# Optimization experiments

Hardware: AMD Instinct MI355X
Metric: run time of the kernel (lower is better)

Reference implementation:

```python
import jax, jax.numpy as jnp
import numpy as np

B, GRID, CIN, COUT, TDIM, NMODES = 32, 128, 32, 32, 256, 32
M = NMODES // 2 + 1  # kept modes per axis = 17
FFT_NORM = 'forward'


def setup_inputs() -> dict:
    key = jax.random.key(0)
    ks = jax.random.split(key, 10)
    w_std = float(np.sqrt(1.0 / (2.0 * CIN)))          # normal_initializer(in_co_dim)
    k_std = float(np.sqrt(1.0 / TDIM))                 # ~lecun_normal for Dense kernels
    wshape = (M, M, CIN, COUT)
    return {
        'x': jax.random.normal(ks[0], (B, GRID, GRID, CIN), jnp.float32),
        't_emb': jax.random.normal(ks[1], (B, TDIM), jnp.float32),
        'w1_real': w_std * jax.random.normal(ks[2], wshape, jnp.float32),
        'w1_imag': w_std * jax.random.normal(ks[3], wshape, jnp.float32),
        'w2_real': w_std * jax.random.normal(ks[4], wshape, jnp.float32),
        'w2_imag': w_std * jax.random.normal(ks[5], wshape, jnp.float32),
        'k1_real': k_std * jax.random.normal(ks[6], (TDIM, M), jnp.float32),
        'k1_imag': k_std * jax.random.normal(ks[7], (TDIM, M), jnp.float32),
        'k2_real': k_std * jax.random.normal(ks[8], (TDIM, M), jnp.float32),
        'k2_imag': k_std * jax.random.normal(ks[9], (TDIM, M), jnp.float32),
    }


def reference(x, t_emb, w1_real, w1_imag, w2_real, w2_imag,
              k1_real, k1_imag, k2_real, k2_imag):
    b, n = x.shape[0], x.shape[1]
    # rFFT2 over spatial axes: (b, n, n//2+1, cin) complex
    x_ft = jnp.fft.rfft2(x, axes=(1, 2), norm=FFT_NORM)

    w1 = w1_real + 1j * w1_imag  # (M, M, cin, cout)
    w2 = w2_real + 1j * w2_imag
    # Time modulation: Dense(no bias) -> complex per-mode scale t[b, i].
    # The original builds diag(t) and einsums it into the weights; that equals a
    # simple broadcast scale over the first mode axis, fused here.
    t1 = (t_emb @ k1_real) + 1j * (t_emb @ k1_imag)  # (b, M)
    t2 = (t_emb @ k2_real) + 1j * (t_emb @ k2_imag)

    # Mode-truncated complex channel contraction, scaled by t along axis i.
    xf1 = jnp.einsum('bijc,ijco->bijo', x_ft[:, :M, :M, :], w1) * t1[:, :, None, None]
    xf2 = jnp.einsum('bijc,ijco->bijo', x_ft[:, -M:, :M, :], w2) * t2[:, :, None, None]

    out_ft = jnp.zeros((b, n, n // 2 + 1, COUT), dtype=jnp.complex64)
    out_ft = out_ft.at[:, :M, :M, :].set(xf1)
    out_ft = out_ft.at[:, -M:, :M, :].set(xf2)

    return jnp.fft.irfft2(out_ft, s=(n, n), axes=(1, 2), norm=FFT_NORM)
```

## Files before the change

kernel.cpp:

```cpp
#include <hip/hip_runtime.h>
#include <stdint.h>


#define TWO_PI_OVER_128 0.04908738521234052f

__global__ __launch_bounds__(128) void k_tproj(
    const float* __restrict__ temb, const float* __restrict__ k1r, const float* __restrict__ k1i,
    const float* __restrict__ k2r, const float* __restrict__ k2i, float* __restrict__ tbuf)
{
    int b = blockIdx.x, tid = threadIdx.x;
    __shared__ float ts[256];
    for (int d = tid; d < 256; d += 128) ts[d] = temb[b * 256 + d];
    __syncthreads();
    if (tid < 68) {
        int which = (tid >= 34) ? 1 : 0;
        int rem = tid - which * 34;
        int i = rem >> 1, part = rem & 1;
        const float* kp = which ? (part ? k2i : k2r) : (part ? k1i : k1r);
        float acc = 0.f;
        for (int d = 0; d < 256; ++d) acc += ts[d] * kp[d * 17 + i];
        tbuf[((which * 32 + b) * 17 + i) * 2 + part] = acc;
    }
}

__global__ __launch_bounds__(64) void k_fwd_y(const float* __restrict__ x, float2* __restrict__ T1)
{
    int blk = blockIdx.x;
    int b = blk >> 7, xr = blk & 127;
    __shared__ float xs[128 * 32];
    int tid = threadIdx.x;
    const float4* xv = (const float4*)(x + ((size_t)blk << 12));
    float4* xs4 = (float4*)xs;
#pragma unroll
    for (int i = 0; i < 16; ++i) xs4[tid + (i << 6)] = xv[tid + (i << 6)];
    __syncthreads();
    for (int i = tid; i < 2016; i += 64) {
        int y = (i >> 5) + 1, c = i & 31;
        float a = xs[(y << 5) + c], q = xs[((128 - y) << 5) + c];
        xs[(y << 5) + c] = a + q;
        xs[((128 - y) << 5) + c] = a - q;
    }
    __syncthreads();
    int jg = tid >> 3, cg = tid & 7, c0 = cg << 2;
    float re[2][4] = {{0,0,0,0},{0,0,0,0}}, im[2][4] = {{0,0,0,0},{0,0,0,0}};
    float stc[2], sts[2], cr[2], ci[2];
#pragma unroll
    for (int t = 0; t < 2; ++t) {
        int j = jg + t * 8;
        float sn, cs; sincosf(TWO_PI_OVER_128 * (float)j, &sn, &cs);
        stc[t] = cs; sts[t] = -sn; cr[t] = cs; ci[t] = -sn;
    }
    for (int y = 1; y <= 63; ++y) {
        float4 s = *(const float4*)&xs[(y << 5) + c0];
        float4 d = *(const float4*)&xs[((128 - y) << 5) + c0];
#pragma unroll
        for (int t = 0; t < 2; ++t) {
            re[t][0] = fmaf(s.x, cr[t], re[t][0]);
            re[t][1] = fmaf(s.y, cr[t], re[t][1]);
            re[t][2] = fmaf(s.z, cr[t], re[t][2]);
            re[t][3] = fmaf(s.w, cr[t], re[t][3]);
            im[t][0] = fmaf(d.x, ci[t], im[t][0]);
            im[t][1] = fmaf(d.y, ci[t], im[t][1]);
            im[t][2] = fmaf(d.z, ci[t], im[t][2]);
            im[t][3] = fmaf(d.w, ci[t], im[t][3]);
            float nr = cr[t] * stc[t] - ci[t] * sts[t];
            ci[t] = fmaf(cr[t], sts[t], ci[t] * stc[t]);
            cr[t] = nr;
        }
    }
    const float s_ = 1.f / 16384.f;
    float x0[4], x64[4];
    *(float4*)x0  = *(const float4*)&xs[c0];
    *(float4*)x64 = *(const float4*)&xs[(64 << 5) + c0];
#pragma unroll
    for (int t = 0; t < 2; ++t) {
        int j = jg + t * 8;
        float sg = (j & 1) ? -1.f : 1.f;
        float2* p = T1 + (((size_t)(b * 17 + j) * 128 + xr) << 5) + c0;
        float4 v0 = make_float4((re[t][0] + x0[0] + sg * x64[0]) * s_, im[t][0] * s_,
                                (re[t][1] + x0[1] + sg * x64[1]) * s_, im[t][1] * s_);
        float4 v1 = make_float4((re[t][2] + x0[2] + sg * x64[2]) * s_, im[t][2] * s_,
                                (re[t][3] + x0[3] + sg * x64[3]) * s_, im[t][3] * s_);
        ((float4*)p)[0] = v0; ((float4*)p)[1] = v1;
    }
    if (jg == 0) {
        float re2[4] = {0,0,0,0}, im2[4] = {0,0,0,0};
        const float cs = 0.7071067811865476f, sn = -0.7071067811865476f;
        float cr2 = cs, ci2 = sn;
        for (int y = 1; y <= 63; ++y) {
            float4 s = *(const float4*)&xs[(y << 5) + c0];
            float4 d = *(const float4*)&xs[((128 - y) << 5) + c0];
            re2[0] = fmaf(s.x, cr2, re2[0]); re2[1] = fmaf(s.y, cr2, re2[1]);
            re2[2] = fmaf(s.z, cr2, re2[2]); re2[3] = fmaf(s.w, cr2, re2[3]);
            im2[0] = fmaf(d.x, ci2, im2[0]); im2[1] = fmaf(d.y, ci2, im2[1]);
            im2[2] = fmaf(d.z, ci2, im2[2]); im2[3] = fmaf(d.w, ci2, im2[3]);
            float nr = cr2 * cs - ci2 * sn;
            ci2 = fmaf(cr2, sn, ci2 * cs);
            cr2 = nr;
        }
        float2* p = T1 + (((size_t)(b * 17 + 16) * 128 + xr) << 5) + c0;
        float4 v0 = make_float4((re2[0] + x0[0] + x64[0]) * s_, im2[0] * s_,
                                (re2[1] + x0[1] + x64[1]) * s_, im2[1] * s_);
        float4 v1 = make_float4((re2[2] + x0[2] + x64[2]) * s_, im2[2] * s_,
                                (re2[3] + x0[3] + x64[3]) * s_, im2[3] * s_);
        ((float4*)p)[0] = v0; ((float4*)p)[1] = v1;
    }
}

__global__ __launch_bounds__(512) void k_mid_fused(
    const float2* __restrict__ T1, const float* __restrict__ w1r, const float* __restrict__ w1i,
    const float* __restrict__ w2r, const float* __restrict__ w2i,
    const float* __restrict__ tbuf, float2* __restrict__ U)
{
    int blk = blockIdx.x;
    int b = blk / 17, j = blk - b * 17;
    __shared__ float4 Ts4[2048];
    __shared__ float2 Xf[34 * 32];
    __shared__ float ct[128], st[128];
    int tid = threadIdx.x;
    const float4* s4 = (const float4*)(T1 + (size_t)blk * 4096);
    for (int i = tid; i < 2048; i += 512) Ts4[i] = s4[i];
    if (tid < 128) {
        float a = TWO_PI_OVER_128 * (float)tid;
        sincosf(a, &st[tid], &ct[tid]);
    }
    __syncthreads();
    for (int i = tid; i < 1008; i += 512) {
        int x = (i >> 4) + 1, cp = i & 15;
        float4 a = Ts4[(x << 4) + cp], q = Ts4[((128 - x) << 4) + cp];
        Ts4[(x << 4) + cp] = make_float4(a.x + q.x, a.y + q.y, a.z + q.z, a.w + q.w);
        Ts4[((128 - x) << 4) + cp] = make_float4(a.x - q.x, a.y - q.y, a.z - q.z, a.w - q.w);
    }
    __syncthreads();
    {
        int cp = tid & 15, g = tid >> 4;
        if (g < 16) {
            int f = g + 1;
            float sn, cs; sincosf(TWO_PI_OVER_128 * (float)f, &sn, &cs);
            float cr = cs, ci = sn;
            float P0=0,Q0=0,R0=0,T0=0,P1=0,Q1=0,R1=0,T1a=0;
            for (int x = 1; x <= 63; ++x) {
                float4 S = Ts4[(x << 4) + cp];
                float4 D = Ts4[((128 - x) << 4) + cp];
                P0 = fmaf(S.x, cr, P0); Q0 = fmaf(D.y, ci, Q0);
                R0 = fmaf(S.y, cr, R0); T0 = fmaf(D.x, ci, T0);
                P1 = fmaf(S.z, cr, P1); Q1 = fmaf(D.w, ci, Q1);
                R1 = fmaf(S.w, cr, R1); T1a = fmaf(D.z, ci, T1a);
                float nr = cr * cs - ci * sn;
                ci = fmaf(cr, sn, ci * cs);
                cr = nr;
            }
            float4 t0 = Ts4[cp], t64 = Ts4[(64 << 4) + cp];
            float sg = (f & 1) ? -1.f : 1.f;
            float b0r = t0.x + sg * t64.x, b0i = t0.y + sg * t64.y;
            float b1r = t0.z + sg * t64.z, b1i = t0.w + sg * t64.w;
            int ia = f, ib = 34 - f;
            Xf[ia * 32 + cp*2]   = make_float2(P0 + Q0 + b0r, R0 - T0 + b0i);
            Xf[ia * 32 + cp*2+1] = make_float2(P1 + Q1 + b1r, R1 - T1a + b1i);
            Xf[ib * 32 + cp*2]   = make_float2(P0 - Q0 + b0r, R0 + T0 + b0i);
            Xf[ib * 32 + cp*2+1] = make_float2(P1 - Q1 + b1r, R1 + T1a + b1i);
            if (g == 0) {
                float A0=0,B0=0,A1=0,B1=0;
                for (int x = 1; x <= 63; ++x) {
                    float4 S = Ts4[(x << 4) + cp];
                    A0 += S.x; B0 += S.y; A1 += S.z; B1 += S.w;
                }
                Xf[cp*2]   = make_float2(A0 + t0.x + t64.x, B0 + t0.y + t64.y);
                Xf[cp*2+1] = make_float2(A1 + t0.z + t64.z, B1 + t0.w + t64.w);
            }
            if (g == 8) {
                float sn2, cs2; sincosf(TWO_PI_OVER_128 * 111.f, &sn2, &cs2);
                float cr2 = cs2, ci2 = sn2;
                float p0=0,q0=0,r0=0,s0=0,p1=0,q1=0,r1=0,s1=0;
                for (int x = 1; x <= 63; ++x) {
                    float4 S = Ts4[(x << 4) + cp];
                    float4 D = Ts4[((128 - x) << 4) + cp];
                    p0 = fmaf(S.x, cr2, p0); q0 = fmaf(D.y, ci2, q0);
                    r0 = fmaf(S.y, cr2, r0); s0 = fmaf(D.x, ci2, s0);
                    p1 = fmaf(S.z, cr2, p1); q1 = fmaf(D.w, ci2, q1);
                    r1 = fmaf(S.w, cr2, r1); s1 = fmaf(D.z, ci2, s1);
                    float nr = cr2 * cs2 - ci2 * sn2;
                    ci2 = fmaf(cr2, sn2, ci2 * cs2);
                    cr2 = nr;
                }
                float c0r = t0.x - t64.x, c0i = t0.y - t64.y;
                float c1r = t0.z - t64.z, c1i = t0.w - t64.w;
                Xf[17*32 + cp*2]   = make_float2(p0 + q0 + c0r, r0 - s0 + c0i);
                Xf[17*32 + cp*2+1] = make_float2(p1 + q1 + c1r, r1 - s1 + c1i);
            }
        }
    }
    __syncthreads();
    float2* Ys = (float2*)Ts4;
    {
        int o = tid & 31, gi = tid >> 5;
#pragma unroll
        for (int t = 0; t < 3; ++t) {
            int ii = gi + (t << 4);
            if (ii < 34) {
                int irow = (ii < 17) ? ii : ii - 17;
                const float* wr = ((ii < 17) ? w1r : w2r) + ((irow * 17 + j) << 10) + o;
                const float* wi = ((ii < 17) ? w1i : w2i) + ((irow * 17 + j) << 10) + o;
                float ar = 0.f, ai = 0.f;
#pragma unroll 8
                for (int c = 0; c < 32; ++c) {
                    float2 xv = Xf[ii * 32 + c];
                    float wre = wr[c << 5], wim = wi[c << 5];
                    ar += xv.x * wre - xv.y * wim;
                    ai += xv.x * wim + xv.y * wre;
                }
                int which = (ii >= 17) ? 1 : 0;
                const float* tp = tbuf + ((which * 32 + b) * 17 + irow) * 2;
                float tr = tp[0], ti = tp[1];
                Ys[ii * 32 + o] = make_float2(ar * tr - ai * ti, ar * ti + ai * tr);
            }
        }
    }
    __syncthreads();
    {
        int o = tid & 31, g = tid >> 5;
        float yr[34], yi[34];
#pragma unroll
        for (int i = 0; i < 34; ++i) { float2 v = Ys[i * 32 + o]; yr[i] = v.x; yi[i] = v.y; }
        float2* Ub = U + ((size_t)b * 128 * 17 + j) * 32 + o;
        if (g == 0) {
            float sr = 0.f, si = 0.f;
#pragma unroll
            for (int i = 0; i < 34; ++i) { sr += yr[i]; si += yi[i]; }
            Ub[0] = make_float2(sr, si);
        }
        for (int k = 0; k < 4; ++k) {
            int x = 1 + g + (k << 4);
            if (x == 64) {
                float sr = 0.f, si = 0.f;
#pragma unroll
                for (int i = 0; i < 34; ++i) {
                    float sg2 = (i & 1) ? -1.f : 1.f;
                    sr = fmaf(sg2, yr[i], sr); si = fmaf(sg2, yi[i], si);
                }
                Ub[(size_t)64 * 544] = make_float2(sr, si);
            } else {
                float cx = ct[x], sx = st[x];
                float A1=0,A2=0,A3=0,A4=0;
                float cr = 1.f, ci = 0.f;
#pragma unroll
                for (int i = 0; i < 17; ++i) {
                    A1 = fmaf(yr[i], cr, A1); A4 = fmaf(yr[i], ci, A4);
                    A3 = fmaf(yi[i], cr, A3); A2 = fmaf(yi[i], ci, A2);
                    float nr = cr * cx - ci * sx;
                    ci = fmaf(cr, sx, ci * cx);
                    cr = nr;
                }
                int k2 = (111 * x) & 127;
                cr = ct[k2]; ci = st[k2];
#pragma unroll
                for (int i = 17; i < 34; ++i) {
                    A1 = fmaf(yr[i], cr, A1); A4 = fmaf(yr[i], ci, A4);
                    A3 = fmaf(yi[i], cr, A3); A2 = fmaf(yi[i], ci, A2);
                    float nr = cr * cx - ci * sx;
                    ci = fmaf(cr, sx, ci * cx);
                    cr = nr;
                }
                Ub[(size_t)x * 544]         = make_float2(A1 - A2, A3 + A4);
                Ub[(size_t)(128 - x) * 544] = make_float2(A1 + A2, A3 - A4);
            }
        }
    }
}

__global__ __launch_bounds__(256) void k_fwd_x_mix(
    const float2* __restrict__ T1, const float* __restrict__ w1r, const float* __restrict__ w1i,
    const float* __restrict__ w2r, const float* __restrict__ w2i,
    const float* __restrict__ tbuf, float2* __restrict__ Y)
{
    int blk = blockIdx.x;
    int b = blk / 17, j = blk - b * 17;
    __shared__ float4 Ts4[2048];
    __shared__ float2 Xf[34 * 32];
    int tid = threadIdx.x;
    const float4* s4 = (const float4*)(T1 + (size_t)blk * 4096);
    for (int i = tid; i < 2048; i += 256) Ts4[i] = s4[i];
    __syncthreads();
    {
        int cp = tid & 15, g = tid >> 4;
        int il[3] = {g, g + 16, g + 32};
        float stc[3], sts[3];
#pragma unroll
        for (int t = 0; t < 3; ++t) {
            int i = il[t];
            int f = (i < 17) ? i : i + 94;
            float a = -TWO_PI_OVER_128 * (float)(f & 127);
            sincosf(a, &sts[t], &stc[t]);
        }
        float cr[3] = {1.f, 1.f, 1.f}, ci[3] = {0.f, 0.f, 0.f};
        float r0[3] = {0,0,0}, i0[3] = {0,0,0}, r1[3] = {0,0,0}, i1[3] = {0,0,0};
        const float4* Tc = Ts4 + cp;
#pragma unroll 2
        for (int xx = 0; xx < 128; ++xx) {
            float4 tv = Tc[xx << 4];
#pragma unroll
            for (int t = 0; t < 3; ++t) {
                r0[t] += tv.x * cr[t] - tv.y * ci[t];
                i0[t] += tv.x * ci[t] + tv.y * cr[t];
                r1[t] += tv.z * cr[t] - tv.w * ci[t];
                i1[t] += tv.z * ci[t] + tv.w * cr[t];
                float nr = cr[t] * stc[t] - ci[t] * sts[t];
                ci[t] = fmaf(cr[t], sts[t], ci[t] * stc[t]);
                cr[t] = nr;
            }
        }
#pragma unroll
        for (int t = 0; t < 3; ++t) {
            int i = il[t];
            if (i < 34) {
                Xf[i * 32 + cp * 2]     = make_float2(r0[t], i0[t]);
                Xf[i * 32 + cp * 2 + 1] = make_float2(r1[t], i1[t]);
            }
        }
    }
    __syncthreads();
    {
        int o = tid & 31, gi = tid >> 5;
#pragma unroll
        for (int t = 0; t < 5; ++t) {
            int ii = gi + (t << 3);
            if (ii < 34) {
                int irow = (ii < 17) ? ii : ii - 17;
                const float* wr = ((ii < 17) ? w1r : w2r) + ((irow * 17 + j) << 10) + o;
                const float* wi = ((ii < 17) ? w1i : w2i) + ((irow * 17 + j) << 10) + o;
                float ar = 0.f, ai = 0.f;
#pragma unroll 8
                for (int cc2 = 0; cc2 < 32; ++cc2) {
                    float2 xv = Xf[ii * 32 + cc2];
                    float wre = wr[cc2 << 5];
                    float wim = wi[cc2 << 5];
                    ar += xv.x * wre - xv.y * wim;
                    ai += xv.x * wim + xv.y * wre;
                }
                int which = (ii >= 17) ? 1 : 0;
                const float* tp = tbuf + ((which * 32 + b) * 17 + irow) * 2;
                float tr = tp[0], ti = tp[1];
                Y[(size_t)blk * (34 * 32) + ii * 32 + o] =
                    make_float2(ar * tr - ai * ti, ar * ti + ai * tr);
            }
        }
    }
}

__global__ __launch_bounds__(256) void k_inv_x(const float2* __restrict__ Y, float2* __restrict__ U)
{
    int blk = blockIdx.x;
    int b = blk / 17, j = blk - b * 17;
    __shared__ float2 Ys[34 * 32];
    __shared__ float ct[128], st[128];
    int tid = threadIdx.x;
    if (tid < 128) {
        float a = TWO_PI_OVER_128 * (float)tid;
        sincosf(a, &st[tid], &ct[tid]);
    }
    const float2* src = Y + (size_t)blk * (34 * 32);
    for (int i = tid; i < 34 * 32; i += 256) Ys[i] = src[i];
    __syncthreads();
    int o = tid & 31, g = tid >> 5;
    float yr[34], yi[34];
#pragma unroll
    for (int i = 0; i < 34; ++i) { float2 v = Ys[i * 32 + o]; yr[i] = v.x; yi[i] = v.y; }
    for (int xi = 0; xi < 16; ++xi) {
        int xr = (xi << 3) + g;
        float cx = ct[xr], sx = st[xr];
        float cr = 1.f, ci = 0.f, re = 0.f, im = 0.f;
#pragma unroll
        for (int i = 0; i < 17; ++i) {
            re += yr[i] * cr - yi[i] * ci;
            im += yr[i] * ci + yi[i] * cr;
            float nr = cr * cx - ci * sx;
            ci = fmaf(cr, sx, ci * cx);
            cr = nr;
        }
        int k2 = (111 * xr) & 127;
        cr = ct[k2]; ci = st[k2];
#pragma unroll
        for (int i = 17; i < 34; ++i) {
            re += yr[i] * cr - yi[i] * ci;
            im += yr[i] * ci + yi[i] * cr;
            float nr = cr * cx - ci * sx;
            ci = fmaf(cr, sx, ci * cx);
            cr = nr;
        }
        U[(((size_t)(b * 128 + xr)) * 17 + j) * 32 + o] = make_float2(re, im);
    }
}

__global__ __launch_bounds__(128) void k_inv_y(const float2* __restrict__ U, float* __restrict__ out)
{
    int blk = blockIdx.x;
    __shared__ float2 Us[17 * 32];
    int tid = threadIdx.x;
    const float4* src4 = (const float4*)(U + (size_t)blk * 544);
    float4* Us4 = (float4*)Us;
    for (int i = tid; i < 272; i += 128) Us4[i] = src4[i];
    __syncthreads();
    int cg = tid & 15, yg = tid >> 4, c0 = cg << 1;
    float base0, base1;
    {
        float4 v = *(const float4*)&Us[c0];
        base0 = v.x; base1 = v.z;
    }
    float urr[16][2], uii[16][2];
#pragma unroll
    for (int j = 1; j <= 16; ++j) {
        float4 v = *(const float4*)&Us[j * 32 + c0];
        urr[j-1][0] = 2.f * v.x; uii[j-1][0] = 2.f * v.y;
        urr[j-1][1] = 2.f * v.z; uii[j-1][1] = 2.f * v.w;
    }
    float* op = out + ((size_t)blk << 12);
    for (int k = 0; k < 9; ++k) {
        int y = yg + (k << 3);
        if (y > 64) break;
        float cy, sy; sincosf(TWO_PI_OVER_128 * (float)y, &sy, &cy);
        float cr = cy, ci = sy;
        float A0 = 0.f, A1 = 0.f, B0 = 0.f, B1 = 0.f;
#pragma unroll
        for (int j = 0; j < 16; ++j) {
            A0 = fmaf(urr[j][0], cr, A0);
            B0 = fmaf(uii[j][0], ci, B0);
            A1 = fmaf(urr[j][1], cr, A1);
            B1 = fmaf(uii[j][1], ci, B1);
            float nr = cr * cy - ci * sy;
            ci = fmaf(cr, sy, ci * cy);
            cr = nr;
        }
        *(float2*)&op[(y << 5) + c0] = make_float2(base0 + A0 - B0, base1 + A1 - B1);
        if (y > 0 && y < 64)
            *(float2*)&op[((128 - y) << 5) + c0] = make_float2(base0 + A0 + B0, base1 + A1 + B1);
    }
}

extern "C" void kernel_launch(void* const* d_in, const int* in_sizes, int n_in,
                              void* d_out, int out_size, void* d_ws, size_t ws_size,
                              hipStream_t stream)
{
    const float* x    = (const float*)d_in[0];
    const float* temb = (const float*)d_in[1];
    const float* w1r  = (const float*)d_in[2];
    const float* w1i  = (const float*)d_in[3];
    const float* w2r  = (const float*)d_in[4];
    const float* w2i  = (const float*)d_in[5];
    const float* k1r  = (const float*)d_in[6];
    const float* k1i  = (const float*)d_in[7];
    const float* k2r  = (const float*)d_in[8];
    const float* k2i  = (const float*)d_in[9];
    float* out = (float*)d_out;

    char* ws = (char*)d_ws;
    const size_t T1_BYTES = 17825792;
    const size_t NEED_FUSED = 2 * T1_BYTES + 8704;

    if (ws_size >= NEED_FUSED) {
        float2* T1 = (float2*)ws;
        float2* U  = (float2*)(ws + T1_BYTES);
        float*  tb = (float*)(ws + 2 * T1_BYTES);
        k_tproj    <<<32,   128, 0, stream>>>(temb, k1r, k1i, k2r, k2i, tb);
        k_fwd_y    <<<4096, 64,  0, stream>>>(x, T1);
        k_mid_fused<<<544,  512, 0, stream>>>(T1, w1r, w1i, w2r, w2i, tb, U);
        k_inv_y    <<<4096, 128, 0, stream>>>(U, out);
    } else {
        float2* T1 = (float2*)ws;
        float2* Yb = (float2*)(ws + T1_BYTES);
        float*  tb = (float*)(ws + T1_BYTES + 4734976);
        float2* U  = T1;
        k_tproj    <<<32,   128, 0, stream>>>(temb, k1r, k1i, k2r, k2i, tb);
        k_fwd_y    <<<4096, 64,  0, stream>>>(x, T1);
        k_fwd_x_mix<<<544,  256, 0, stream>>>(T1, w1r, w1i, w2r, w2i, tb, Yb);
        k_inv_x    <<<544,  256, 0, stream>>>(Yb, U);
        k_inv_y    <<<4096, 128, 0, stream>>>(U, out);
    }
}
```

Before: 213.0 us.

## Replace y-axis DFT stages with split-bf16 MFMA matrix multiplies against precomputed twiddle tables

Rewrites the forward and inverse y-axis DFT kernels as small GEMMs on MFMA units. Twiddle matrices are precomputed into bf16 hi/lo tables by a new single-block kernel, and three-term split-bf16 products approximate fp32 accuracy. The fallback path with separate x-mix and inverse-x kernels is removed, so a larger workspace is now always assumed. The aim is to move the scalar FMA recurrence work onto matrix cores, at the cost of an extra launch, table reads and some precision loss from the bf16 splitting.

Measured after the change: 213.7 us. No clear change (+0.3%).

```diff
diff --git a/kernel.cpp b/kernel.cpp
--- a/kernel.cpp
+++ b/kernel.cpp
@@ -2,7 +2,19 @@
 #include <stdint.h>
 
 
+typedef unsigned int uint32;
+typedef __attribute__((ext_vector_type(8))) short short8;
+typedef __attribute__((ext_vector_type(4))) float f32x4;
+
 #define TWO_PI_OVER_128 0.04908738521234052f
+
+__device__ __forceinline__ unsigned short bfhi(float v) {
+    uint32 u = __float_as_uint(v);
+    return (unsigned short)((u + 0x7fffu + ((u >> 16) & 1u)) >> 16);
+}
+__device__ __forceinline__ float bf2f(unsigned short h) {
+    return __uint_as_float(((uint32)h) << 16);
+}
 
 __global__ __launch_bounds__(128) void k_tproj(
     const float* __restrict__ temb, const float* __restrict__ k1r, const float* __restrict__ k1i,
@@ -23,87 +35,150 @@
     }
 }
 
-__global__ __launch_bounds__(64) void k_fwd_y(const float* __restrict__ x, float2* __restrict__ T1)
-{
-    int blk = blockIdx.x;
-    int b = blk >> 7, xr = blk & 127;
-    __shared__ float xs[128 * 32];
+__global__ __launch_bounds__(256) void k_mktab(
+    unsigned short* __restrict__ Dhi, unsigned short* __restrict__ Dlo,
+    unsigned short* __restrict__ Ehi, unsigned short* __restrict__ Elo,
+    float* __restrict__ Et)
+{
     int tid = threadIdx.x;
-    const float4* xv = (const float4*)(x + ((size_t)blk << 12));
-    float4* xs4 = (float4*)xs;
-#pragma unroll
-    for (int i = 0; i < 16; ++i) xs4[tid + (i << 6)] = xv[tid + (i << 6)];
-    __syncthreads();
-    for (int i = tid; i < 2016; i += 64) {
-        int y = (i >> 5) + 1, c = i & 31;
-        float a = xs[(y << 5) + c], q = xs[((128 - y) << 5) + c];
-        xs[(y << 5) + c] = a + q;
-        xs[((128 - y) << 5) + c] = a - q;
-    }
-    __syncthreads();
-    int jg = tid >> 3, cg = tid & 7, c0 = cg << 2;
-    float re[2][4] = {{0,0,0,0},{0,0,0,0}}, im[2][4] = {{0,0,0,0},{0,0,0,0}};
-    float stc[2], sts[2], cr[2], ci[2];
-#pragma unroll
-    for (int t = 0; t < 2; ++t) {
-        int j = jg + t * 8;
-        float sn, cs; sincosf(TWO_PI_OVER_128 * (float)j, &sn, &cs);
-        stc[t] = cs; sts[t] = -sn; cr[t] = cs; ci[t] = -sn;
-    }
-    for (int y = 1; y <= 63; ++y) {
-        float4 s = *(const float4*)&xs[(y << 5) + c0];
-        float4 d = *(const float4*)&xs[((128 - y) << 5) + c0];
-#pragma unroll
-        for (int t = 0; t < 2; ++t) {
-            re[t][0] = fmaf(s.x, cr[t], re[t][0]);
-            re[t][1] = fmaf(s.y, cr[t], re[t][1]);
-            re[t][2] = fmaf(s.z, cr[t], re[t][2]);
-            re[t][3] = fmaf(s.w, cr[t], re[t][3]);
-            im[t][0] = fmaf(d.x, ci[t], im[t][0]);
-            im[t][1] = fmaf(d.y, ci[t], im[t][1]);
-            im[t][2] = fmaf(d.z, ci[t], im[t][2]);
-            im[t][3] = fmaf(d.w, ci[t], im[t][3]);
-            float nr = cr[t] * stc[t] - ci[t] * sts[t];
-            ci[t] = fmaf(cr[t], sts[t], ci[t] * stc[t]);
-            cr[t] = nr;
-        }
-    }
-    const float s_ = 1.f / 16384.f;
-    float x0[4], x64[4];
-    *(float4*)x0  = *(const float4*)&xs[c0];
-    *(float4*)x64 = *(const float4*)&xs[(64 << 5) + c0];
-#pragma unroll
-    for (int t = 0; t < 2; ++t) {
-        int j = jg + t * 8;
-        float sg = (j & 1) ? -1.f : 1.f;
-        float2* p = T1 + (((size_t)(b * 17 + j) * 128 + xr) << 5) + c0;
-        float4 v0 = make_float4((re[t][0] + x0[0] + sg * x64[0]) * s_, im[t][0] * s_,
-                                (re[t][1] + x0[1] + sg * x64[1]) * s_, im[t][1] * s_);
-        float4 v1 = make_float4((re[t][2] + x0[2] + sg * x64[2]) * s_, im[t][2] * s_,
-                                (re[t][3] + x0[3] + sg * x64[3]) * s_, im[t][3] * s_);
-        ((float4*)p)[0] = v0; ((float4*)p)[1] = v1;
-    }
-    if (jg == 0) {
-        float re2[4] = {0,0,0,0}, im2[4] = {0,0,0,0};
-        const float cs = 0.7071067811865476f, sn = -0.7071067811865476f;
-        float cr2 = cs, ci2 = sn;
-        for (int y = 1; y <= 63; ++y) {
-            float4 s = *(const float4*)&xs[(y << 5) + c0];
-            float4 d = *(const float4*)&xs[((128 - y) << 5) + c0];
-            re2[0] = fmaf(s.x, cr2, re2[0]); re2[1] = fmaf(s.y, cr2, re2[1]);
-            re2[2] = fmaf(s.z, cr2, re2[2]); re2[3] = fmaf(s.w, cr2, re2[3]);
-            im2[0] = fmaf(d.x, ci2, im2[0]); im2[1] = fmaf(d.y, ci2, im2[1]);
-            im2[2] = fmaf(d.z, ci2, im2[2]); im2[3] = fmaf(d.w, ci2, im2[3]);
-            float nr = cr2 * cs - ci2 * sn;
-            ci2 = fmaf(cr2, sn, ci2 * cs);
-            cr2 = nr;
-        }
-        float2* p = T1 + (((size_t)(b * 17 + 16) * 128 + xr) << 5) + c0;
-        float4 v0 = make_float4((re2[0] + x0[0] + x64[0]) * s_, im2[0] * s_,
-                                (re2[1] + x0[1] + x64[1]) * s_, im2[1] * s_);
-        float4 v1 = make_float4((re2[2] + x0[2] + x64[2]) * s_, im2[2] * s_,
-                                (re2[3] + x0[3] + x64[3]) * s_, im2[3] * s_);
-        ((float4*)p)[0] = v0; ((float4*)p)[1] = v1;
+    for (int i = tid; i < 48 * 128; i += 256) {
+        int m = i >> 7, y = i & 127;
+        float v = 0.f;
+        if (m < 34) {
+            int p = m >> 1;
+            int k = (p * y) & 127;
+            float sn, cs; sincosf(TWO_PI_OVER_128 * (float)k, &sn, &cs);
+            v = ((m & 1) ? -sn : cs) * (1.f / 16384.f);
+        }
+        unsigned short h = bfhi(v);
+        Dhi[i] = h; Dlo[i] = bfhi(v - bf2f(h));
+    }
+    for (int i = tid; i < 128 * 32; i += 256) {
+        int y = i >> 5, q = i & 31;
+        int j = q >> 1;
+        int k = (j * y) & 127;
+        float sn, cs; sincosf(TWO_PI_OVER_128 * (float)k, &sn, &cs);
+        float w = (j == 0) ? 1.f : 2.f;
+        float v = (q & 1) ? (-w * sn) : (w * cs);
+        if (q == 1) v = 0.f;
+        unsigned short h = bfhi(v);
+        Ehi[i] = h; Elo[i] = bfhi(v - bf2f(h));
+    }
+    for (int i = tid; i < 128; i += 256) {
+        int k = (16 * i) & 127;
+        float sn, cs; sincosf(TWO_PI_OVER_128 * (float)k, &sn, &cs);
+        Et[i * 2] = 2.f * cs; Et[i * 2 + 1] = -2.f * sn;
+    }
+}
+
+__global__ __launch_bounds__(256) void k_fwd_y_mfma(
+    const float* __restrict__ x, float2* __restrict__ T1,
+    const unsigned short* __restrict__ Dhi, const unsigned short* __restrict__ Dlo)
+{
+    int wave = threadIdx.x >> 6, lane = threadIdx.x & 63;
+    int row = (blockIdx.x << 2) + wave;
+    int b = row >> 7, xr = row & 127;
+    const float* xp = x + ((size_t)row << 12);
+    int col = lane & 15, quad = lane >> 4;
+    f32x4 acc[3][2];
+#pragma unroll
+    for (int m = 0; m < 3; ++m)
+#pragma unroll
+        for (int n = 0; n < 2; ++n) acc[m][n] = (f32x4){0.f, 0.f, 0.f, 0.f};
+#pragma unroll
+    for (int t = 0; t < 4; ++t) {
+        int y0 = t * 32 + quad * 8;
+        short8 xh[2], xl[2];
+#pragma unroll
+        for (int n = 0; n < 2; ++n) {
+            const float* xc = xp + (n << 4) + col;
+#pragma unroll
+            for (int jj = 0; jj < 8; ++jj) {
+                float v = xc[(y0 + jj) << 5];
+                unsigned short h = bfhi(v);
+                xh[n][jj] = (short)h;
+                xl[n][jj] = (short)bfhi(v - bf2f(h));
+            }
+        }
+#pragma unroll
+        for (int m = 0; m < 3; ++m) {
+            int doff = (((m << 4) + col) << 7) + t * 32 + quad * 8;
+            short8 dh = *(const short8*)(Dhi + doff);
+            short8 dl = *(const short8*)(Dlo + doff);
+#pragma unroll
+            for (int n = 0; n < 2; ++n) {
+                acc[m][n] = __builtin_amdgcn_mfma_f32_16x16x32_bf16(dh, xh[n], acc[m][n], 0, 0, 0);
+                acc[m][n] = __builtin_amdgcn_mfma_f32_16x16x32_bf16(dh, xl[n], acc[m][n], 0, 0, 0);
+                acc[m][n] = __builtin_amdgcn_mfma_f32_16x16x32_bf16(dl, xh[n], acc[m][n], 0, 0, 0);
+            }
+        }
+    }
+#pragma unroll
+    for (int m = 0; m < 3; ++m) {
+        int j0 = (m << 3) + (quad << 1);
+#pragma unroll
+        for (int n = 0; n < 2; ++n) {
+            int c = (n << 4) + col;
+            if (m < 2 || quad == 0) {
+                float2* p = T1 + (((size_t)(b * 17 + j0) * 128 + xr) << 5) + c;
+                *p = make_float2(acc[m][n][0], acc[m][n][1]);
+            }
+            if (m < 2) {
+                float2* p = T1 + (((size_t)(b * 17 + j0 + 1) * 128 + xr) << 5) + c;
+                *p = make_float2(acc[m][n][2], acc[m][n][3]);
+            }
+        }
+    }
+}
+
+__global__ __launch_bounds__(256) void k_inv_y_mfma(
+    const float2* __restrict__ U, float* __restrict__ out,
+    const unsigned short* __restrict__ Ehi, const unsigned short* __restrict__ Elo,
+    const float* __restrict__ Et)
+{
+    int wave = threadIdx.x >> 6, lane = threadIdx.x & 63;
+    int row = (blockIdx.x << 2) + wave;
+    const float2* Up = U + (size_t)row * 544;
+    float* outp = out + ((size_t)row << 12);
+    int col = lane & 15, quad = lane >> 4;
+    short8 uh[2], ul[2];
+#pragma unroll
+    for (int n = 0; n < 2; ++n) {
+        int o = (n << 4) + col;
+#pragma unroll
+        for (int m = 0; m < 4; ++m) {
+            int j = (quad << 2) + m;
+            float2 uv = Up[(j << 5) + o];
+            unsigned short h0 = bfhi(uv.x);
+            uh[n][2 * m]     = (short)h0;
+            ul[n][2 * m]     = (short)bfhi(uv.x - bf2f(h0));
+            unsigned short h1 = bfhi(uv.y);
+            uh[n][2 * m + 1] = (short)h1;
+            ul[n][2 * m + 1] = (short)bfhi(uv.y - bf2f(h1));
+        }
+    }
+    float2 u16a = Up[(16 << 5) + col];
+    float2 u16b = Up[(16 << 5) + 16 + col];
+#pragma unroll
+    for (int mt = 0; mt < 8; ++mt) {
+        f32x4 a0 = (f32x4){0.f, 0.f, 0.f, 0.f};
+        f32x4 a1 = (f32x4){0.f, 0.f, 0.f, 0.f};
+        int eoff = (((mt << 4) + col) << 5) + (quad << 3);
+        short8 eh = *(const short8*)(Ehi + eoff);
+        short8 el = *(const short8*)(Elo + eoff);
+        a0 = __builtin_amdgcn_mfma_f32_16x16x32_bf16(eh, uh[0], a0, 0, 0, 0);
+        a0 = __builtin_amdgcn_mfma_f32_16x16x32_bf16(eh, ul[0], a0, 0, 0, 0);
+        a0 = __builtin_amdgcn_mfma_f32_16x16x32_bf16(el, uh[0], a0, 0, 0, 0);
+        a1 = __builtin_amdgcn_mfma_f32_16x16x32_bf16(eh, uh[1], a1, 0, 0, 0);
+        a1 = __builtin_amdgcn_mfma_f32_16x16x32_bf16(eh, ul[1], a1, 0, 0, 0);
+        a1 = __builtin_amdgcn_mfma_f32_16x16x32_bf16(el, uh[1], a1, 0, 0, 0);
+#pragma unroll
+        for (int r = 0; r < 4; ++r) {
+            int y = (mt << 4) + (quad << 2) + r;
+            float e0 = Et[y << 1], e1 = Et[(y << 1) + 1];
+            outp[(y << 5) + col]      = a0[r] + u16a.x * e0 + u16a.y * e1;
+            outp[(y << 5) + 16 + col] = a1[r] + u16b.x * e0 + u16b.y * e1;
+        }
     }
 }
 
@@ -268,174 +343,6 @@
     }
 }
 
-__global__ __launch_bounds__(256) void k_fwd_x_mix(
-    const float2* __restrict__ T1, const float* __restrict__ w1r, const float* __restrict__ w1i,
-    const float* __restrict__ w2r, const float* __restrict__ w2i,
-    const float* __restrict__ tbuf, float2* __restrict__ Y)
-{
-    int blk = blockIdx.x;
-    int b = blk / 17, j = blk - b * 17;
-    __shared__ float4 Ts4[2048];
-    __shared__ float2 Xf[34 * 32];
-    int tid = threadIdx.x;
-    const float4* s4 = (const float4*)(T1 + (size_t)blk * 4096);
-    for (int i = tid; i < 2048; i += 256) Ts4[i] = s4[i];
-    __syncthreads();
-    {
-        int cp = tid & 15, g = tid >> 4;
-        int il[3] = {g, g + 16, g + 32};
-        float stc[3], sts[3];
-#pragma unroll
-        for (int t = 0; t < 3; ++t) {
-            int i = il[t];
-            int f = (i < 17) ? i : i + 94;
-            float a = -TWO_PI_OVER_128 * (float)(f & 127);
-            sincosf(a, &sts[t], &stc[t]);
-        }
-        float cr[3] = {1.f, 1.f, 1.f}, ci[3] = {0.f, 0.f, 0.f};
-        float r0[3] = {0,0,0}, i0[3] = {0,0,0}, r1[3] = {0,0,0}, i1[3] = {0,0,0};
-        const float4* Tc = Ts4 + cp;
-#pragma unroll 2
-        for (int xx = 0; xx < 128; ++xx) {
-            float4 tv = Tc[xx << 4];
-#pragma unroll
-            for (int t = 0; t < 3; ++t) {
-                r0[t] += tv.x * cr[t] - tv.y * ci[t];
-                i0[t] += tv.x * ci[t] + tv.y * cr[t];
-                r1[t] += tv.z * cr[t] - tv.w * ci[t];
-                i1[t] += tv.z * ci[t] + tv.w * cr[t];
-                float nr = cr[t] * stc[t] - ci[t] * sts[t];
-                ci[t] = fmaf(cr[t], sts[t], ci[t] * stc[t]);
-                cr[t] = nr;
-            }
-        }
-#pragma unroll
-        for (int t = 0; t < 3; ++t) {
-            int i = il[t];
-            if (i < 34) {
-                Xf[i * 32 + cp * 2]     = make_float2(r0[t], i0[t]);
-                Xf[i * 32 + cp * 2 + 1] = make_float2(r1[t], i1[t]);
-            }
-        }
-    }
-    __syncthreads();
-    {
-        int o = tid & 31, gi = tid >> 5;
-#pragma unroll
-        for (int t = 0; t < 5; ++t) {
-            int ii = gi + (t << 3);
-            if (ii < 34) {
-                int irow = (ii < 17) ? ii : ii - 17;
-                const float* wr = ((ii < 17) ? w1r : w2r) + ((irow * 17 + j) << 10) + o;
-                const float* wi = ((ii < 17) ? w1i : w2i) + ((irow * 17 + j) << 10) + o;
-                float ar = 0.f, ai = 0.f;
-#pragma unroll 8
-                for (int cc2 = 0; cc2 < 32; ++cc2) {
-                    float2 xv = Xf[ii * 32 + cc2];
-                    float wre = wr[cc2 << 5];
-                    float wim = wi[cc2 << 5];
-                    ar += xv.x * wre - xv.y * wim;
-                    ai += xv.x * wim + xv.y * wre;
-                }
-                int which = (ii >= 17) ? 1 : 0;
-                const float* tp = tbuf + ((which * 32 + b) * 17 + irow) * 2;
-                float tr = tp[0], ti = tp[1];
-                Y[(size_t)blk * (34 * 32) + ii * 32 + o] =
-                    make_float2(ar * tr - ai * ti, ar * ti + ai * tr);
-            }
-        }
-    }
-}
-
-__global__ __launch_bounds__(256) void k_inv_x(const float2* __restrict__ Y, float2* __restrict__ U)
-{
-    int blk = blockIdx.x;
-    int b = blk / 17, j = blk - b * 17;
-    __shared__ float2 Ys[34 * 32];
-    __shared__ float ct[128], st[128];
-    int tid = threadIdx.x;
-    if (tid < 128) {
-        float a = TWO_PI_OVER_128 * (float)tid;
-        sincosf(a, &st[tid], &ct[tid]);
-    }
-    const float2* src = Y + (size_t)blk * (34 * 32);
-    for (int i = tid; i < 34 * 32; i += 256) Ys[i] = src[i];
-    __syncthreads();
-    int o = tid & 31, g = tid >> 5;
-    float yr[34], yi[34];
-#pragma unroll
-    for (int i = 0; i < 34; ++i) { float2 v = Ys[i * 32 + o]; yr[i] = v.x; yi[i] = v.y; }
-    for (int xi = 0; xi < 16; ++xi) {
-        int xr = (xi << 3) + g;
-        float cx = ct[xr], sx = st[xr];
-        float cr = 1.f, ci = 0.f, re = 0.f, im = 0.f;
-#pragma unroll
-        for (int i = 0; i < 17; ++i) {
-            re += yr[i] * cr - yi[i] * ci;
-            im += yr[i] * ci + yi[i] * cr;
-            float nr = cr * cx - ci * sx;
-            ci = fmaf(cr, sx, ci * cx);
-            cr = nr;
-        }
-        int k2 = (111 * xr) & 127;
-        cr = ct[k2]; ci = st[k2];
-#pragma unroll
-        for (int i = 17; i < 34; ++i) {
-            re += yr[i] * cr - yi[i] * ci;
-            im += yr[i] * ci + yi[i] * cr;
-            float nr = cr * cx - ci * sx;
-            ci = fmaf(cr, sx, ci * cx);
-            cr = nr;
-        }
-        U[(((size_t)(b * 128 + xr)) * 17 + j) * 32 + o] = make_float2(re, im);
-    }
-}
-
-__global__ __launch_bounds__(128) void k_inv_y(const float2* __restrict__ U, float* __restrict__ out)
-{
-    int blk = blockIdx.x;
-    __shared__ float2 Us[17 * 32];
-    int tid = threadIdx.x;
-    const float4* src4 = (const float4*)(U + (size_t)blk * 544);
-    float4* Us4 = (float4*)Us;
-    for (int i = tid; i < 272; i += 128) Us4[i] = src4[i];
-    __syncthreads();
-    int cg = tid & 15, yg = tid >> 4, c0 = cg << 1;
-    float base0, base1;
-    {
-        float4 v = *(const float4*)&Us[c0];
-        base0 = v.x; base1 = v.z;
-    }
-    float urr[16][2], uii[16][2];
-#pragma unroll
-    for (int j = 1; j <= 16; ++j) {
-        float4 v = *(const float4*)&Us[j * 32 + c0];
-        urr[j-1][0] = 2.f * v.x; uii[j-1][0] = 2.f * v.y;
-        urr[j-1][1] = 2.f * v.z; uii[j-1][1] = 2.f * v.w;
-    }
-    float* op = out + ((size_t)blk << 12);
-    for (int k = 0; k < 9; ++k) {
-        int y = yg + (k << 3);
-        if (y > 64) break;
-        float cy, sy; sincosf(TWO_PI_OVER_128 * (float)y, &sy, &cy);
-        float cr = cy, ci = sy;
-        float A0 = 0.f, A1 = 0.f, B0 = 0.f, B1 = 0.f;
-#pragma unroll
-        for (int j = 0; j < 16; ++j) {
-            A0 = fmaf(urr[j][0], cr, A0);
-            B0 = fmaf(uii[j][0], ci, B0);
-            A1 = fmaf(urr[j][1], cr, A1);
-            B1 = fmaf(uii[j][1], ci, B1);
-            float nr = cr * cy - ci * sy;
-            ci = fmaf(cr, sy, ci * cy);
-            cr = nr;
-        }
-        *(float2*)&op[(y << 5) + c0] = make_float2(base0 + A0 - B0, base1 + A1 - B1);
-        if (y > 0 && y < 64)
-            *(float2*)&op[((128 - y) << 5) + c0] = make_float2(base0 + A0 + B0, base1 + A1 + B1);
-    }
-}
-
 extern "C" void kernel_launch(void* const* d_in, const int* in_sizes, int n_in,
                               void* d_out, int out_size, void* d_ws, size_t ws_size,
                               hipStream_t stream)
@@ -453,26 +360,19 @@
     float* out = (float*)d_out;
 
     char* ws = (char*)d_ws;
-    const size_t T1_BYTES = 17825792;
-    const size_t NEED_FUSED = 2 * T1_BYTES + 8704;
-
-    if (ws_size >= NEED_FUSED) {
-        float2* T1 = (float2*)ws;
-        float2* U  = (float2*)(ws + T1_BYTES);
-        float*  tb = (float*)(ws + 2 * T1_BYTES);
-        k_tproj    <<<32,   128, 0, stream>>>(temb, k1r, k1i, k2r, k2i, tb);
-        k_fwd_y    <<<4096, 64,  0, stream>>>(x, T1);
-        k_mid_fused<<<544,  512, 0, stream>>>(T1, w1r, w1i, w2r, w2i, tb, U);
-        k_inv_y    <<<4096, 128, 0, stream>>>(U, out);
-    } else {
-        float2* T1 = (float2*)ws;
-        float2* Yb = (float2*)(ws + T1_BYTES);
-        float*  tb = (float*)(ws + T1_BYTES + 4734976);
-        float2* U  = T1;
-        k_tproj    <<<32,   128, 0, stream>>>(temb, k1r, k1i, k2r, k2i, tb);
-        k_fwd_y    <<<4096, 64,  0, stream>>>(x, T1);
-        k_fwd_x_mix<<<544,  256, 0, stream>>>(T1, w1r, w1i, w2r, w2i, tb, Yb);
-        k_inv_x    <<<544,  256, 0, stream>>>(Yb, U);
-        k_inv_y    <<<4096, 128, 0, stream>>>(U, out);
-    }
-}
+    const size_t T1_B = 17825792;
+    float2* T1 = (float2*)ws;
+    float2* U  = (float2*)(ws + T1_B);
+    float*  tb = (float*)(ws + 2 * T1_B);
+    unsigned short* Dhi = (unsigned short*)(ws + 2 * T1_B + 8704);
+    unsigned short* Dlo = (unsigned short*)(ws + 2 * T1_B + 8704 + 12288);
+    unsigned short* Ehi = (unsigned short*)(ws + 2 * T1_B + 8704 + 24576);
+    unsigned short* Elo = (unsigned short*)(ws + 2 * T1_B + 8704 + 24576 + 8192);
+    float* Et = (float*)(ws + 2 * T1_B + 8704 + 24576 + 16384);
+
+    k_mktab     <<<1,    256, 0, stream>>>(Dhi, Dlo, Ehi, Elo, Et);
+    k_tproj     <<<32,   128, 0, stream>>>(temb, k1r, k1i, k2r, k2i, tb);
+    k_fwd_y_mfma<<<1024, 256, 0, stream>>>(x, T1, Dhi, Dlo);
+    k_mid_fused <<<544,  512, 0, stream>>>(T1, w1r, w1i, w2r, w2i, tb, U);
+    k_inv_y_mfma<<<1024, 256, 0, stream>>>(U, out, Ehi, Elo, Et);
+}
```
